# Kernel optimization log

Measured on AMD Instinct MI355X. Metric: run time of the kernel, lower is better.

Reference implementation:

```python
import jax, jax.numpy as jnp
import numpy as np
from jax import lax

K = 9      # 3x3 kernel points
PAD = 1
EPS = 1e-5

def _conv3x3(x, w):
    # x: [B,C,H,W], w: [O,C,3,3] -> [B,O,H,W], stride 1, pad 1
    return lax.conv_general_dilated(x, w, (1, 1), [(PAD, PAD), (PAD, PAD)],
                                    dimension_numbers=('NCHW', 'OIHW', 'NCHW'))

def _bilinear_sample(x, py, px):
    # x: [B,C,H,W]; py,px: [B,K,H,W] float sample coords -> [B,C,K,H,W]
    # Zero padding outside bounds (mmcv deform_conv semantics).
    B, C, H, W = x.shape
    y0 = jnp.floor(py)
    x0 = jnp.floor(px)
    wy1 = py - y0
    wx1 = px - x0
    xf = x.reshape(B, C, H * W)

    def corner(yc, xc, wgt):
        valid = (yc >= 0) & (yc <= H - 1) & (xc >= 0) & (xc <= W - 1)
        yi = jnp.clip(yc, 0, H - 1).astype(jnp.int32)
        xi = jnp.clip(xc, 0, W - 1).astype(jnp.int32)
        idx = (yi * W + xi).reshape(B, -1)                       # [B, K*H*W]
        v = jax.vmap(lambda f, i: jnp.take(f, i, axis=1))(xf, idx)  # [B,C,K*H*W]
        v = v.reshape(B, C, K, H, W)
        return v * jnp.where(valid, wgt, 0.0)[:, None]

    return (corner(y0,     x0,     (1 - wy1) * (1 - wx1))
          + corner(y0,     x0 + 1, (1 - wy1) * wx1)
          + corner(y0 + 1, x0,     wy1 * (1 - wx1))
          + corner(y0 + 1, x0 + 1, wy1 * wx1))

def _dcn_bn_relu(x, w_off, b_off, w, gamma, beta, mean, var):
    B, C, H, W = x.shape
    # offset conv: [B, 2K, H, W]; channel pairs are (dy, dx) per kernel point
    off = _conv3x3(x, w_off) + b_off[None, :, None, None]
    off = off.reshape(B, K, 2, H, W)
    dy, dx = off[:, :, 0], off[:, :, 1]
    kk = jnp.arange(K)
    ky = (kk // 3 - PAD).astype(x.dtype)   # kernel y deltas
    kx = (kk % 3 - PAD).astype(x.dtype)    # kernel x deltas
    py = dy + jnp.arange(H, dtype=x.dtype)[None, None, :, None] + ky[None, :, None, None]
    px = dx + jnp.arange(W, dtype=x.dtype)[None, None, None, :] + kx[None, :, None, None]
    s = _bilinear_sample(x, py, px)                       # [B,C,K,H,W]
    out = jnp.einsum('bckhw,ock->bohw', s, w.reshape(w.shape[0], C, K))
    # BatchNorm (eval stats) + ReLU
    inv = gamma * lax.rsqrt(var + EPS)
    return jax.nn.relu(out * inv[None, :, None, None]
                       + (beta - mean * inv)[None, :, None, None])

def setup_inputs() -> dict:
    key = jax.random.key(0)
    ks = jax.random.split(key, 8)
    B, Cin, Cout, H, W = 4, 64, 64, 128, 128
    fan = 1.0 / np.sqrt(Cin * K)
    return {
        'x':      jax.random.normal(ks[0], (B, Cin, H, W), jnp.float32),
        'w_off1': jax.random.normal(ks[1], (2 * K, Cin, 3, 3), jnp.float32) * 0.1,
        'b_off1': jnp.zeros((2 * K,), jnp.float32),
        'w1':     jax.random.normal(ks[2], (Cout, Cin, 3, 3), jnp.float32) * fan,
        'g1':     jnp.ones((Cout,), jnp.float32),
        'be1':    jnp.zeros((Cout,), jnp.float32),
        'm1':     jax.random.normal(ks[3], (Cout,), jnp.float32) * 0.01,
        'v1':     jnp.abs(jax.random.normal(ks[4], (Cout,), jnp.float32)) * 0.1 + 0.9,
        'w_off2': jax.random.normal(ks[5], (2 * K, Cout, 3, 3), jnp.float32) * 0.1,
        'b_off2': jnp.zeros((2 * K,), jnp.float32),
        'w2':     jax.random.normal(ks[6], (Cout, Cout, 3, 3), jnp.float32) * fan,
        'g2':     jnp.ones((Cout,), jnp.float32),
        'be2':    jnp.zeros((Cout,), jnp.float32),
        'm2':     jax.random.normal(ks[7], (Cout,), jnp.float32) * 0.01,
        'v2':     jnp.ones((Cout,), jnp.float32),
    }

def reference(x, w_off1, b_off1, w1, g1, be1, m1, v1,
              w_off2, b_off2, w2, g2, be2, m2, v2):
    h = _dcn_bn_relu(x, w_off1, b_off1, w1, g1, be1, m1, v1)
    return _dcn_bn_relu(h, w_off2, b_off2, w2, g2, be2, m2, v2)
```

## Files before the change

kernel.cpp:

```cpp
#include <hip/hip_runtime.h>

#define BAR_LGKM()                                         \
  do {                                                     \
    asm volatile("s_waitcnt lgkmcnt(0)" ::: "memory");     \
    __builtin_amdgcn_s_barrier();                          \
  } while (0)

__device__ __forceinline__ int swz_block(int bid) {
  return ((bid & 7) << 7) + (bid >> 3);
}


__global__ __launch_bounds__(256) void prep_kernel(
    const float* __restrict__ w1, const float* __restrict__ w2,
    const float* __restrict__ woff1, const float* __restrict__ woff2,
    const float* __restrict__ g1, const float* __restrict__ be1,
    const float* __restrict__ m1, const float* __restrict__ v1,
    const float* __restrict__ g2, const float* __restrict__ be2,
    const float* __restrict__ m2, const float* __restrict__ v2,
    float* __restrict__ ws) {
  float* wt1 = ws;
  float* wt2 = ws + 36864;
  float* wo1 = ws + 73728;
  float* wo2 = ws + 84096;
  float* bn1 = ws + 94464;
  float* bn2 = ws + 94592;
  int idx = blockIdx.x * 256 + threadIdx.x;
  if (idx < 73728) {
    int t = (idx < 36864) ? idx : idx - 36864;
    const float* w = (idx < 36864) ? w1 : w2;
    float* wt = (idx < 36864) ? wt1 : wt2;
    int oi = t & 7;
    int rest = t >> 3;
    int k = rest % 9;
    int cog = rest / 9;
    int og = cog & 7, c = cog >> 3;
    int o = og * 8 + oi;
    wt[t] = w[(o * 64 + c) * 9 + k];
  } else if (idx < 94464) {
    int u = idx - 73728;
    int t2 = (u < 10368) ? u : u - 10368;
    const float* w = (u < 10368) ? woff1 : woff2;
    float* wo = (u < 10368) ? wo1 : wo2;
    int j = t2 % 18;
    int v = t2 / 18;
    int tt = v % 9;
    int c = v / 9;
    wo[t2] = w[(j * 64 + c) * 9 + tt];
  } else if (idx < 94528) {
    int o = idx - 94464;
    float s = g1[o] * rsqrtf(v1[o] + 1e-5f);
    bn1[o] = s;
    bn1[64 + o] = be1[o] - m1[o] * s;
  } else if (idx < 94592) {
    int o = idx - 94528;
    float s = g2[o] * rsqrtf(v2[o] + 1e-5f);
    bn2[o] = s;
    bn2[64 + o] = be2[o] - m2[o] * s;
  }
}

__global__ __launch_bounds__(512, 8) void conv_off_kernel(
    const float* __restrict__ xin, const float* __restrict__ wofft,
    const float* __restrict__ boff, float* __restrict__ off) {
  __shared__ float halo[2][792];
  int tid = threadIdx.x;
  int pxl = tid & 63;
  int og = tid >> 6;
  int ogu = __builtin_amdgcn_readfirstlane(og);
  int p0 = swz_block(blockIdx.x) * 64;
  int b = p0 >> 14, hw0 = p0 & 16383;
  int h = hw0 >> 7, w0 = hw0 & 127;

  bool sv = tid < 396;
  int pp = (tid >= 198) ? 1 : 0;
  int pos = tid - pp * 198;
  int r = pos / 66, cc = pos - r * 66;
  int yy = h + r - 1, xx = w0 + cc - 1;
  bool inb = sv && (yy >= 0) && (yy < 128) && (xx >= 0) && (xx < 128);
  int ofs = (yy << 7) + xx;
  const float* xb0 = xin + ((size_t)(b * 64) << 14);

  float stg0 = inb ? xb0[((size_t)pp << 14) + ofs] : 0.f;
  float stg1 = inb ? xb0[((size_t)(2 + pp) << 14) + ofs] : 0.f;

  int jbase = (ogu < 2) ? ogu * 3 : 6 + (ogu - 2) * 2;
  int nj = (ogu < 2) ? 3 : 2;
  int jc2 = jbase + 2;
  if (jc2 > 17) jc2 = 17;

  float acc[3] = {0.f, 0.f, 0.f};

#pragma unroll 1
  for (int cg = 0; cg < 64; cg += 4) {
    int bufi = (cg >> 2) & 1;
    if (sv) {
      halo[bufi][pp * 198 + pos] = stg0;
      halo[bufi][(2 + pp) * 198 + pos] = stg1;
    }
    if (cg < 60) {
      stg0 = inb ? xb0[((size_t)(cg + 4 + pp) << 14) + ofs] : 0.f;
      stg1 = inb ? xb0[((size_t)(cg + 6 + pp) << 14) + ofs] : 0.f;
    }
    BAR_LGKM();
    const float* hb = halo[bufi];
#pragma unroll
    for (int p = 0; p < 4; ++p) {
      const float* wc = wofft + (cg + p) * 162;
#pragma unroll
      for (int t = 0; t < 9; ++t) {
        float v = hb[p * 198 + (t / 3) * 66 + pxl + (t % 3)];
        acc[0] = fmaf(v, wc[t * 18 + jbase], acc[0]);
        acc[1] = fmaf(v, wc[t * 18 + jbase + 1], acc[1]);
        acc[2] = fmaf(v, wc[t * 18 + jc2], acc[2]);
      }
    }
  }
#pragma unroll
  for (int i = 0; i < 3; ++i) {
    if (i < nj) {
      int j = jbase + i;
      off[((size_t)(b * 18 + j) << 14) + hw0 + pxl] = acc[i] + boff[j];
    }
  }
}

__global__ __launch_bounds__(512, 8) void dcn_main_kernel(
    const float* __restrict__ xin, const float* __restrict__ off,
    const float* __restrict__ wt, const float* __restrict__ bn,
    float* __restrict__ out) {
  __shared__ float sbuf[2][576];
  int tid = threadIdx.x;
  int pxl = tid & 63;
  int og = tid >> 6;
  int ogu = __builtin_amdgcn_readfirstlane(og);
  int p0 = swz_block(blockIdx.x) * 64;
  int b = p0 >> 14, hw0 = p0 & 16383;
  int h = hw0 >> 7, w0 = hw0 & 127;
  const float* xb = xin + ((size_t)b << 20);

  bool act1 = (tid & 7) == 0;
  int s1 = 512 + (tid >> 3);

  float q[2][4];
  const float* pa[2];
  const float* pb[2];

#pragma unroll
  for (int j = 0; j < 2; ++j) {
    bool a = (j == 0) || act1;
    int s = (j == 0) ? tid : s1;
    int k = s >> 6;
    int pxs = s & 63;
    int hw = hw0 + pxs;
    float dy = a ? off[((size_t)(b * 18 + 2 * k) << 14) + hw] : 0.f;
    float dx = a ? off[((size_t)(b * 18 + 2 * k + 1) << 14) + hw] : 0.f;
    float py = (float)(h + k / 3 - 1) + dy;
    float pxf = (float)(w0 + pxs + k % 3 - 1) + dx;
    float y0f = floorf(py), x0f = floorf(pxf);
    float wy1 = py - y0f, wx1 = pxf - x0f;
    float wy0 = 1.f - wy1, wx0 = 1.f - wx1;
    int y0 = (int)y0f, x0 = (int)x0f;
    int y1 = y0 + 1, x1 = x0 + 1;
    bool vy0 = (y0 >= 0) && (y0 <= 127);
    bool vy1 = (y1 >= 0) && (y1 <= 127);
    bool vx0 = (x0 >= 0) && (x0 <= 127);
    bool vx1 = (x1 >= 0) && (x1 <= 127);
    float pw0 = (vy0 && vx0) ? wy0 * wx0 : 0.f;
    float pw1 = (vy0 && vx1) ? wy0 * wx1 : 0.f;
    float pw2 = (vy1 && vx0) ? wy1 * wx0 : 0.f;
    float pw3 = (vy1 && vx1) ? wy1 * wx1 : 0.f;
    int y0c = min(max(y0, 0), 127), y1c = min(max(y1, 0), 127);
    int xb2 = min(max(x0, 0), 126);
    bool se0 = (x0 == xb2);
    bool se1 = (x0 + 1 == xb2);
    q[j][0] = (se0 ? pw0 : 0.f) + (se1 ? pw1 : 0.f);
    q[j][1] = (se0 ? 0.f : pw0) + (se1 ? 0.f : pw1);
    q[j][2] = (se0 ? pw2 : 0.f) + (se1 ? pw3 : 0.f);
    q[j][3] = (se0 ? 0.f : pw2) + (se1 ? 0.f : pw3);
    pa[j] = xb + ((y0c << 7) + xb2);
    pb[j] = xb + ((y1c << 7) + xb2);
  }

  float2 t0a = *(const float2*)pa[0];
  float2 t1a = *(const float2*)pb[0];
  float2 t0b = act1 ? *(const float2*)pa[1] : make_float2(0.f, 0.f);
  float2 t1b = act1 ? *(const float2*)pb[1] : make_float2(0.f, 0.f);
  pa[0] += 16384; pb[0] += 16384; pa[1] += 16384; pb[1] += 16384;

  float acc[8];
#pragma unroll
  for (int oi = 0; oi < 8; ++oi) acc[oi] = 0.f;

#pragma unroll 1
  for (int c = 0; c < 64; ++c) {
    sbuf[c & 1][tid] = fmaf(q[0][0], t0a.x,
                       fmaf(q[0][1], t0a.y,
                       fmaf(q[0][2], t1a.x, q[0][3] * t1a.y)));
    if (act1) {
      sbuf[c & 1][s1] = fmaf(q[1][0], t0b.x,
                        fmaf(q[1][1], t0b.y,
                        fmaf(q[1][2], t1b.x, q[1][3] * t1b.y)));
    }
    if (c < 63) {
      t0a = *(const float2*)pa[0];
      t1a = *(const float2*)pb[0];
      if (act1) {
        t0b = *(const float2*)pa[1];
        t1b = *(const float2*)pb[1];
      }
      pa[0] += 16384; pb[0] += 16384; pa[1] += 16384; pb[1] += 16384;
    }
    BAR_LGKM();
    const float* wc = wt + (c * 8 + ogu) * 72;
#pragma unroll
    for (int k = 0; k < 9; ++k) {
      float sval = sbuf[c & 1][k * 64 + pxl];
#pragma unroll
      for (int oi = 0; oi < 8; ++oi)
        acc[oi] = fmaf(sval, wc[k * 8 + oi], acc[oi]);
    }
  }

#pragma unroll
  for (int oi = 0; oi < 8; ++oi) {
    int o = ogu * 8 + oi;
    float rres = fmaf(acc[oi], bn[o], bn[64 + o]);
    out[((size_t)(b * 64 + o) << 14) + hw0 + pxl] = fmaxf(rres, 0.f);
  }
}

extern "C" void kernel_launch(void* const* d_in, const int* in_sizes, int n_in,
                              void* d_out, int out_size, void* d_ws, size_t ws_size,
                              hipStream_t stream) {
  const float* x      = (const float*)d_in[0];
  const float* w_off1 = (const float*)d_in[1];
  const float* b_off1 = (const float*)d_in[2];
  const float* w1     = (const float*)d_in[3];
  const float* g1     = (const float*)d_in[4];
  const float* be1    = (const float*)d_in[5];
  const float* m1     = (const float*)d_in[6];
  const float* v1     = (const float*)d_in[7];
  const float* w_off2 = (const float*)d_in[8];
  const float* b_off2 = (const float*)d_in[9];
  const float* w2     = (const float*)d_in[10];
  const float* g2     = (const float*)d_in[11];
  const float* be2    = (const float*)d_in[12];
  const float* m2     = (const float*)d_in[13];
  const float* v2     = (const float*)d_in[14];
  float* out = (float*)d_out;

  float* ws   = (float*)d_ws;
  float* wt1  = ws;
  float* wt2  = ws + 36864;
  float* wo1  = ws + 73728;
  float* wo2  = ws + 84096;
  float* bn1  = ws + 94464;
  float* bn2  = ws + 94592;
  float* offb = ws + 94720;
  float* hbuf = ws + 1274368;

  prep_kernel<<<370, 256, 0, stream>>>(w1, w2, w_off1, w_off2,
                                       g1, be1, m1, v1, g2, be2, m2, v2, ws);

  conv_off_kernel<<<1024, 512, 0, stream>>>(x, wo1, b_off1, offb);
  dcn_main_kernel<<<1024, 512, 0, stream>>>(x, offb, wt1, bn1, hbuf);

  conv_off_kernel<<<1024, 512, 0, stream>>>(hbuf, wo2, b_off2, offb);
  dcn_main_kernel<<<1024, 512, 0, stream>>>(hbuf, offb, wt2, bn2, out);
}
```

Baseline: 375.5 us.

## Stage input halo tile in LDS and software-pipeline sampling with weight accumulation

Each block now cooperatively loads a 17x80 halo window of the current input channel into double-buffered shared memory. Bilinear corner values are read from LDS when the sample lies inside the window, and from global memory only when it falls outside. The loop is also restructured so the FMA accumulation for channel c-1 overlaps the sampling for channel c, with one barrier per iteration. This replaces scattered global gathers with coalesced loads, at the cost of more LDS per block, lower launch-bound occupancy, and divergent fallback loads when offsets are large.

```diff
diff --git a/kernel.cpp b/kernel.cpp
--- a/kernel.cpp
+++ b/kernel.cpp
@@ -125,10 +125,11 @@
   }
 }
 
-__global__ __launch_bounds__(512, 8) void dcn_main_kernel(
+__global__ __launch_bounds__(512, 6) void dcn_main_kernel(
     const float* __restrict__ xin, const float* __restrict__ off,
     const float* __restrict__ wt, const float* __restrict__ bn,
     float* __restrict__ out) {
+  __shared__ float xs[2][1360];
   __shared__ float sbuf[2][576];
   int tid = threadIdx.x;
   int pxl = tid & 63;
@@ -142,15 +143,29 @@
   bool act1 = (tid & 7) == 0;
   int s1 = 512 + (tid >> 3);
 
-  float q[2][4];
-  const float* pa[2];
-  const float* pb[2];
+  int h0 = h - 8, xlo = w0 - 8;
+
+  int sofs[3]; bool svld[3];
+#pragma unroll
+  for (int i = 0; i < 3; ++i) {
+    int e = tid + i * 512;
+    int r = e / 80, col = e - r * 80;
+    int y = h0 + r, xc = xlo + col;
+    svld[i] = (e < 1360) && (y >= 0) && (y < 128) && (xc >= 0) && (xc < 128);
+    sofs[i] = (y << 7) + xc;
+  }
+
+  float qa[2][2], qb[2][2];
+  int lA[2], lB[2];
+  int ra[2], rb[2];
+  bool ina[2], inb[2];
 
 #pragma unroll
   for (int j = 0; j < 2; ++j) {
     bool a = (j == 0) || act1;
     int s = (j == 0) ? tid : s1;
     int k = s >> 6;
+    if (k > 8) k = 8;
     int pxs = s & 63;
     int hw = hw0 + pxs;
     float dy = a ? off[((size_t)(b * 18 + 2 * k) << 14) + hw] : 0.f;
@@ -174,51 +189,97 @@
     int xb2 = min(max(x0, 0), 126);
     bool se0 = (x0 == xb2);
     bool se1 = (x0 + 1 == xb2);
-    q[j][0] = (se0 ? pw0 : 0.f) + (se1 ? pw1 : 0.f);
-    q[j][1] = (se0 ? 0.f : pw0) + (se1 ? 0.f : pw1);
-    q[j][2] = (se0 ? pw2 : 0.f) + (se1 ? pw3 : 0.f);
-    q[j][3] = (se0 ? 0.f : pw2) + (se1 ? 0.f : pw3);
-    pa[j] = xb + ((y0c << 7) + xb2);
-    pb[j] = xb + ((y1c << 7) + xb2);
-  }
-
-  float2 t0a = *(const float2*)pa[0];
-  float2 t1a = *(const float2*)pb[0];
-  float2 t0b = act1 ? *(const float2*)pa[1] : make_float2(0.f, 0.f);
-  float2 t1b = act1 ? *(const float2*)pb[1] : make_float2(0.f, 0.f);
-  pa[0] += 16384; pb[0] += 16384; pa[1] += 16384; pb[1] += 16384;
+    float f0 = (se0 ? pw0 : 0.f) + (se1 ? pw1 : 0.f);
+    float f1 = (se0 ? 0.f : pw0) + (se1 ? 0.f : pw1);
+    float f2 = (se0 ? pw2 : 0.f) + (se1 ? pw3 : 0.f);
+    float f3 = (se0 ? 0.f : pw2) + (se1 ? 0.f : pw3);
+    int ry = y0 - h0, rx = x0 - xlo;
+    bool inx = (rx >= 0) && (rx <= 78);
+    bool iA = inx && (ry >= 0) && (ry <= 16);
+    bool iB = inx && (ry >= -1) && (ry <= 15);
+    int la = ry * 80 + rx;
+    lA[j] = min(max(la, 0), 1358);
+    lB[j] = min(max(la + 80, 0), 1358);
+    ina[j] = iA;
+    inb[j] = iB;
+    qa[j][0] = iA ? pw0 : f0;  qa[j][1] = iA ? pw1 : f1;
+    qb[j][0] = iB ? pw2 : f2;  qb[j][1] = iB ? pw3 : f3;
+    ra[j] = (y0c << 7) + xb2;
+    rb[j] = (y1c << 7) + xb2;
+  }
+
+  {
+    float a0 = svld[0] ? xb[sofs[0]] : 0.f;
+    float a1 = svld[1] ? xb[sofs[1]] : 0.f;
+    float a2 = svld[2] ? xb[sofs[2]] : 0.f;
+    xs[0][tid] = a0;
+    xs[0][tid + 512] = a1;
+    if (tid < 336) xs[0][tid + 1024] = a2;
+  }
 
   float acc[8];
 #pragma unroll
   for (int oi = 0; oi < 8; ++oi) acc[oi] = 0.f;
+
+  BAR_LGKM();
 
 #pragma unroll 1
   for (int c = 0; c < 64; ++c) {
-    sbuf[c & 1][tid] = fmaf(q[0][0], t0a.x,
-                       fmaf(q[0][1], t0a.y,
-                       fmaf(q[0][2], t1a.x, q[0][3] * t1a.y)));
+    int buf = c & 1;
+    const float* xp = xb + ((size_t)c << 14);
+    float n0 = 0.f, n1 = 0.f, n2 = 0.f;
+    if (c < 63) {
+      const float* xq = xp + 16384;
+      n0 = svld[0] ? xq[sofs[0]] : 0.f;
+      n1 = svld[1] ? xq[sofs[1]] : 0.f;
+      n2 = svld[2] ? xq[sofs[2]] : 0.f;
+    }
+    const float* xsb = xs[buf];
+    {
+      float vax = xsb[lA[0]], vay = xsb[lA[0] + 1];
+      float vbx = xsb[lB[0]], vby = xsb[lB[0] + 1];
+      if (!ina[0]) { float2 t = *(const float2*)(xp + ra[0]); vax = t.x; vay = t.y; }
+      if (!inb[0]) { float2 t = *(const float2*)(xp + rb[0]); vbx = t.x; vby = t.y; }
+      sbuf[buf][tid] = fmaf(qa[0][0], vax, fmaf(qa[0][1], vay,
+                        fmaf(qb[0][0], vbx, qb[0][1] * vby)));
+    }
     if (act1) {
-      sbuf[c & 1][s1] = fmaf(q[1][0], t0b.x,
-                        fmaf(q[1][1], t0b.y,
-                        fmaf(q[1][2], t1b.x, q[1][3] * t1b.y)));
+      float vax = xsb[lA[1]], vay = xsb[lA[1] + 1];
+      float vbx = xsb[lB[1]], vby = xsb[lB[1] + 1];
+      if (!ina[1]) { float2 t = *(const float2*)(xp + ra[1]); vax = t.x; vay = t.y; }
+      if (!inb[1]) { float2 t = *(const float2*)(xp + rb[1]); vbx = t.x; vby = t.y; }
+      sbuf[buf][s1] = fmaf(qa[1][0], vax, fmaf(qa[1][1], vay,
+                       fmaf(qb[1][0], vbx, qb[1][1] * vby)));
+    }
+    if (c > 0) {
+      const float* wc = wt + ((c - 1) * 8 + ogu) * 72;
+      const float* sb = sbuf[buf ^ 1];
+#pragma unroll
+      for (int k = 0; k < 9; ++k) {
+        float sv_ = sb[k * 64 + pxl];
+#pragma unroll
+        for (int oi = 0; oi < 8; ++oi)
+          acc[oi] = fmaf(sv_, wc[k * 8 + oi], acc[oi]);
+      }
     }
     if (c < 63) {
-      t0a = *(const float2*)pa[0];
-      t1a = *(const float2*)pb[0];
-      if (act1) {
-        t0b = *(const float2*)pa[1];
-        t1b = *(const float2*)pb[1];
-      }
-      pa[0] += 16384; pb[0] += 16384; pa[1] += 16384; pb[1] += 16384;
+      float* xd = xs[buf ^ 1];
+      xd[tid] = n0;
+      xd[tid + 512] = n1;
+      if (tid < 336) xd[tid + 1024] = n2;
     }
     BAR_LGKM();
-    const float* wc = wt + (c * 8 + ogu) * 72;
+  }
+
+  {
+    const float* wc = wt + (63 * 8 + ogu) * 72;
+    const float* sb = sbuf[1];
 #pragma unroll
     for (int k = 0; k < 9; ++k) {
-      float sval = sbuf[c & 1][k * 64 + pxl];
+      float sv_ = sb[k * 64 + pxl];
 #pragma unroll
       for (int oi = 0; oi < 8; ++oi)
-        acc[oi] = fmaf(sval, wc[k * 8 + oi], acc[oi]);
+        acc[oi] = fmaf(sv_, wc[k * 8 + oi], acc[oi]);
     }
   }
 
```

After: 469.7 us. 25.1% more time.

## Use split-bf16 MFMA for deformable conv GEMM instead of scalar FMA

Applied to the files above, without the earlier changes.

The main DCN kernel's channel-by-kernel-point reduction moves from per-thread scalar FMAs to bf16 MFMA 16x16x32 instructions. Both the sampled activations and the weights are split into high and low bf16 parts, and three MFMAs (hi*hi, hi*lo, lo*hi) recover near-fp32 accuracy. The prep kernel repacks weights into an MFMA-friendly hi/lo bf16 layout padded from 9 to 16 per channel. Two channels are packed per K=32 step with double-buffered LDS. The cost is the padding waste and the extra split arithmetic, plus a lower occupancy hint.

```diff
diff --git a/kernel.cpp b/kernel.cpp
--- a/kernel.cpp
+++ b/kernel.cpp
@@ -5,6 +5,11 @@
     asm volatile("s_waitcnt lgkmcnt(0)" ::: "memory");     \
     __builtin_amdgcn_s_barrier();                          \
   } while (0)
+
+typedef __attribute__((ext_vector_type(8))) short bf16x8;
+typedef __attribute__((ext_vector_type(4))) float f32x4;
+typedef unsigned short u16;
+typedef unsigned int u32;
 
 __device__ __forceinline__ int swz_block(int bid) {
   return ((bid & 7) << 7) + (bid >> 3);
@@ -19,26 +24,38 @@
     const float* __restrict__ g2, const float* __restrict__ be2,
     const float* __restrict__ m2, const float* __restrict__ v2,
     float* __restrict__ ws) {
-  float* wt1 = ws;
-  float* wt2 = ws + 36864;
-  float* wo1 = ws + 73728;
-  float* wo2 = ws + 84096;
-  float* bn1 = ws + 94464;
-  float* bn2 = ws + 94592;
+  u16* wm1 = (u16*)ws;
+  u16* wm2 = (u16*)(ws + 65536);
+  float* wo1 = ws + 131072;
+  float* wo2 = ws + 141440;
+  float* bn1 = ws + 151808;
+  float* bn2 = ws + 151936;
   int idx = blockIdx.x * 256 + threadIdx.x;
-  if (idx < 73728) {
-    int t = (idx < 36864) ? idx : idx - 36864;
-    const float* w = (idx < 36864) ? w1 : w2;
-    float* wt = (idx < 36864) ? wt1 : wt2;
-    int oi = t & 7;
-    int rest = t >> 3;
-    int k = rest % 9;
-    int cog = rest / 9;
-    int og = cog & 7, c = cog >> 3;
-    int o = og * 8 + oi;
-    wt[t] = w[(o * 64 + c) * 9 + k];
-  } else if (idx < 94464) {
-    int u = idx - 73728;
+  if (idx < 131072) {
+    int t = idx & 65535;
+    const float* w = (idx < 65536) ? w1 : w2;
+    u16* wm = (idx < 65536) ? wm1 : wm2;
+    int i = t & 7;
+    int lane = (t >> 3) & 63;
+    int nt = (t >> 9) & 3;
+    int pair = t >> 11;
+    int k = ((lane >> 4) << 3) + i;
+    int c = (pair << 1) + (k >> 4);
+    int kk = k & 15;
+    int o = (nt << 4) + (lane & 15);
+    float val = (kk < 9) ? w[(o * 64 + c) * 9 + kk] : 0.f;
+    u32 u = __float_as_uint(val);
+    u32 r = u + 0x7FFFu + ((u >> 16) & 1u);
+    u16 hi = (u16)(r >> 16);
+    float lo = val - __uint_as_float(((u32)hi) << 16);
+    u32 u2 = __float_as_uint(lo);
+    u32 r2 = u2 + 0x7FFFu + ((u2 >> 16) & 1u);
+    u16 lov = (u16)(r2 >> 16);
+    size_t base = ((size_t)(pair * 4 + nt) * 2) * 512 + lane * 8 + i;
+    wm[base] = hi;
+    wm[base + 512] = lov;
+  } else if (idx < 151808) {
+    int u = idx - 131072;
     int t2 = (u < 10368) ? u : u - 10368;
     const float* w = (u < 10368) ? woff1 : woff2;
     float* wo = (u < 10368) ? wo1 : wo2;
@@ -47,13 +64,13 @@
     int tt = v % 9;
     int c = v / 9;
     wo[t2] = w[(j * 64 + c) * 9 + tt];
-  } else if (idx < 94528) {
-    int o = idx - 94464;
+  } else if (idx < 151872) {
+    int o = idx - 151808;
     float s = g1[o] * rsqrtf(v1[o] + 1e-5f);
     bn1[o] = s;
     bn1[64 + o] = be1[o] - m1[o] * s;
-  } else if (idx < 94592) {
-    int o = idx - 94528;
+  } else if (idx < 151936) {
+    int o = idx - 151872;
     float s = g2[o] * rsqrtf(v2[o] + 1e-5f);
     bn2[o] = s;
     bn2[64 + o] = be2[o] - m2[o] * s;
@@ -125,22 +142,26 @@
   }
 }
 
-__global__ __launch_bounds__(512, 8) void dcn_main_kernel(
+__global__ __launch_bounds__(512, 6) void dcn_main_kernel(
     const float* __restrict__ xin, const float* __restrict__ off,
-    const float* __restrict__ wt, const float* __restrict__ bn,
+    const float* __restrict__ wmf, const float* __restrict__ bn,
     float* __restrict__ out) {
-  __shared__ float sbuf[2][576];
+  __shared__ __align__(16) u16 Ah[2][64][40];
+  __shared__ __align__(16) u16 Al[2][64][40];
+  __shared__ __align__(16) u16 Bs[2][4096];
   int tid = threadIdx.x;
-  int pxl = tid & 63;
-  int og = tid >> 6;
-  int ogu = __builtin_amdgcn_readfirstlane(og);
+  int lane = tid & 63;
+  int wv = tid >> 6;
+  int wvu = __builtin_amdgcn_readfirstlane(wv);
   int p0 = swz_block(blockIdx.x) * 64;
   int b = p0 >> 14, hw0 = p0 & 16383;
   int h = hw0 >> 7, w0 = hw0 & 127;
   const float* xb = xin + ((size_t)b << 20);
+  const u16* wmu = (const u16*)wmf;
 
   bool act1 = (tid & 7) == 0;
   int s1 = 512 + (tid >> 3);
+  int px1 = tid >> 3;
 
   float q[2][4];
   const float* pa[2];
@@ -182,25 +203,54 @@
     pb[j] = xb + ((y1c << 7) + xb2);
   }
 
+  for (int z = tid; z < 3584; z += 512) {
+    int m = z / 896;
+    int rr = z - m * 896;
+    int px = rr / 14, jj = rr - (rr / 14) * 14;
+    int k = (jj < 7) ? (9 + jj) : (18 + jj);
+    u16* bp = (m < 2) ? &Ah[m][0][0] : &Al[m - 2][0][0];
+    bp[px * 40 + k] = 0;
+  }
+
   float2 t0a = *(const float2*)pa[0];
   float2 t1a = *(const float2*)pb[0];
   float2 t0b = act1 ? *(const float2*)pa[1] : make_float2(0.f, 0.f);
   float2 t1b = act1 ? *(const float2*)pb[1] : make_float2(0.f, 0.f);
   pa[0] += 16384; pb[0] += 16384; pa[1] += 16384; pb[1] += 16384;
 
-  float acc[8];
-#pragma unroll
-  for (int oi = 0; oi < 8; ++oi) acc[oi] = 0.f;
+  int mt = wvu >> 1;
+  int ntb = (wvu & 1) * 2;
+  int apx = mt * 16 + (lane & 15);
+  int akf = (lane >> 4) * 8;
+
+  f32x4 acc0 = {0.f, 0.f, 0.f, 0.f};
+  f32x4 acc1 = {0.f, 0.f, 0.f, 0.f};
+  uint4 bst = make_uint4(0, 0, 0, 0);
 
 #pragma unroll 1
   for (int c = 0; c < 64; ++c) {
-    sbuf[c & 1][tid] = fmaf(q[0][0], t0a.x,
-                       fmaf(q[0][1], t0a.y,
-                       fmaf(q[0][2], t1a.x, q[0][3] * t1a.y)));
+    int pbW = (c >> 1) & 1;
+    int kh = (c & 1) << 4;
+    {
+      float s = fmaf(q[0][0], t0a.x, fmaf(q[0][1], t0a.y,
+                fmaf(q[0][2], t1a.x, q[0][3] * t1a.y)));
+      u32 u = __float_as_uint(s);
+      Ah[pbW][lane][kh + wv] = (u16)(u >> 16);
+      float lo = s - __uint_as_float(u & 0xFFFF0000u);
+      Al[pbW][lane][kh + wv] = (u16)(__float_as_uint(lo) >> 16);
+    }
     if (act1) {
-      sbuf[c & 1][s1] = fmaf(q[1][0], t0b.x,
-                        fmaf(q[1][1], t0b.y,
-                        fmaf(q[1][2], t1b.x, q[1][3] * t1b.y)));
+      float s = fmaf(q[1][0], t0b.x, fmaf(q[1][1], t0b.y,
+                fmaf(q[1][2], t1b.x, q[1][3] * t1b.y)));
+      u32 u = __float_as_uint(s);
+      Ah[pbW][px1][kh + 8] = (u16)(u >> 16);
+      float lo = s - __uint_as_float(u & 0xFFFF0000u);
+      Al[pbW][px1][kh + 8] = (u16)(__float_as_uint(lo) >> 16);
+    }
+    if (!(c & 1)) {
+      bst = *(const uint4*)(wmu + (size_t)(c >> 1) * 4096 + tid * 8);
+    } else {
+      *(uint4*)&Bs[pbW][tid * 8] = bst;
     }
     if (c < 63) {
       t0a = *(const float2*)pa[0];
@@ -212,21 +262,33 @@
       pa[0] += 16384; pb[0] += 16384; pa[1] += 16384; pb[1] += 16384;
     }
     BAR_LGKM();
-    const float* wc = wt + (c * 8 + ogu) * 72;
-#pragma unroll
-    for (int k = 0; k < 9; ++k) {
-      float sval = sbuf[c & 1][k * 64 + pxl];
-#pragma unroll
-      for (int oi = 0; oi < 8; ++oi)
-        acc[oi] = fmaf(sval, wc[k * 8 + oi], acc[oi]);
-    }
-  }
-
-#pragma unroll
-  for (int oi = 0; oi < 8; ++oi) {
-    int o = ogu * 8 + oi;
-    float rres = fmaf(acc[oi], bn[o], bn[64 + o]);
-    out[((size_t)(b * 64 + o) << 14) + hw0 + pxl] = fmaxf(rres, 0.f);
+    if (c & 1) {
+      bf16x8 ah = *(const bf16x8*)&Ah[pbW][apx][akf];
+      bf16x8 al = *(const bf16x8*)&Al[pbW][apx][akf];
+      const u16* bsp = &Bs[pbW][0];
+      bf16x8 b0h = *(const bf16x8*)(bsp + (ntb * 2 + 0) * 512 + lane * 8);
+      bf16x8 b0l = *(const bf16x8*)(bsp + (ntb * 2 + 1) * 512 + lane * 8);
+      bf16x8 b1h = *(const bf16x8*)(bsp + (ntb * 2 + 2) * 512 + lane * 8);
+      bf16x8 b1l = *(const bf16x8*)(bsp + (ntb * 2 + 3) * 512 + lane * 8);
+      acc0 = __builtin_amdgcn_mfma_f32_16x16x32_bf16(ah, b0h, acc0, 0, 0, 0);
+      acc1 = __builtin_amdgcn_mfma_f32_16x16x32_bf16(ah, b1h, acc1, 0, 0, 0);
+      acc0 = __builtin_amdgcn_mfma_f32_16x16x32_bf16(ah, b0l, acc0, 0, 0, 0);
+      acc1 = __builtin_amdgcn_mfma_f32_16x16x32_bf16(ah, b1l, acc1, 0, 0, 0);
+      acc0 = __builtin_amdgcn_mfma_f32_16x16x32_bf16(al, b0h, acc0, 0, 0, 0);
+      acc1 = __builtin_amdgcn_mfma_f32_16x16x32_bf16(al, b1h, acc1, 0, 0, 0);
+    }
+  }
+
+  int o0 = ntb * 16 + (lane & 15);
+  int prow = mt * 16 + ((lane >> 4) << 2);
+  float sc0 = bn[o0], sh0 = bn[64 + o0];
+  float sc1 = bn[16 + o0], sh1 = bn[80 + o0];
+  float* ob0 = out + (((size_t)(b * 64 + o0)) << 14) + hw0 + prow;
+  float* ob1 = out + (((size_t)(b * 64 + o0 + 16)) << 14) + hw0 + prow;
+#pragma unroll
+  for (int r = 0; r < 4; ++r) {
+    ob0[r] = fmaxf(fmaf(acc0[r], sc0, sh0), 0.f);
+    ob1[r] = fmaxf(fmaf(acc1[r], sc1, sh1), 0.f);
   }
 }
 
@@ -251,21 +313,21 @@
   float* out = (float*)d_out;
 
   float* ws   = (float*)d_ws;
-  float* wt1  = ws;
-  float* wt2  = ws + 36864;
-  float* wo1  = ws + 73728;
-  float* wo2  = ws + 84096;
-  float* bn1  = ws + 94464;
-  float* bn2  = ws + 94592;
-  float* offb = ws + 94720;
-  float* hbuf = ws + 1274368;
-
-  prep_kernel<<<370, 256, 0, stream>>>(w1, w2, w_off1, w_off2,
+  float* wm1  = ws;
+  float* wm2  = ws + 65536;
+  float* wo1  = ws + 131072;
+  float* wo2  = ws + 141440;
+  float* bn1  = ws + 151808;
+  float* bn2  = ws + 151936;
+  float* offb = ws + 152064;
+  float* hbuf = ws + 1331712;
+
+  prep_kernel<<<594, 256, 0, stream>>>(w1, w2, w_off1, w_off2,
                                        g1, be1, m1, v1, g2, be2, m2, v2, ws);
 
   conv_off_kernel<<<1024, 512, 0, stream>>>(x, wo1, b_off1, offb);
-  dcn_main_kernel<<<1024, 512, 0, stream>>>(x, offb, wt1, bn1, hbuf);
+  dcn_main_kernel<<<1024, 512, 0, stream>>>(x, offb, wm1, bn1, hbuf);
 
   conv_off_kernel<<<1024, 512, 0, stream>>>(hbuf, wo2, b_off2, offb);
-  dcn_main_kernel<<<1024, 512, 0, stream>>>(hbuf, offb, wt2, bn2, out);
-}
+  dcn_main_kernel<<<1024, 512, 0, stream>>>(hbuf, offb, wm2, bn2, out);
+}
```

New measurement: 392.8 us. +4.6%, slower.

## Bucket-sort deformable sample points by source row to coalesce gathers

Applied to the files above, without the earlier changes.

Before the channel loop, the kernel stages per-sample bilinear coefficients and indices in shared memory. It then builds a histogram of source rows, relative to the output row, and uses a counting sort to reassign sample points to threads. Threads in a wavefront then gather from nearby rows, which should improve cache-line coalescing of the per-channel gathers, and results are written back to the original sbuf slot. The cost is extra LDS (about 16 KB), atomics and several block barriers, which may reduce occupancy under the 8-blocks launch bound.

```diff
diff --git a/kernel.cpp b/kernel.cpp
--- a/kernel.cpp
+++ b/kernel.cpp
@@ -129,6 +129,9 @@
     const float* __restrict__ xin, const float* __restrict__ off,
     const float* __restrict__ wt, const float* __restrict__ bn,
     float* __restrict__ out) {
+  __shared__ float prm[576 * 6];
+  __shared__ int sortmap[576];
+  __shared__ int hist[32];
   __shared__ float sbuf[2][576];
   int tid = threadIdx.x;
   int pxl = tid & 63;
@@ -142,10 +145,9 @@
   bool act1 = (tid & 7) == 0;
   int s1 = 512 + (tid >> 3);
 
-  float q[2][4];
-  const float* pa[2];
-  const float* pb[2];
-
+  if (tid < 32) hist[tid] = 0;
+
+  int bkt[2];
 #pragma unroll
   for (int j = 0; j < 2; ++j) {
     bool a = (j == 0) || act1;
@@ -174,12 +176,57 @@
     int xb2 = min(max(x0, 0), 126);
     bool se0 = (x0 == xb2);
     bool se1 = (x0 + 1 == xb2);
-    q[j][0] = (se0 ? pw0 : 0.f) + (se1 ? pw1 : 0.f);
-    q[j][1] = (se0 ? 0.f : pw0) + (se1 ? 0.f : pw1);
-    q[j][2] = (se0 ? pw2 : 0.f) + (se1 ? pw3 : 0.f);
-    q[j][3] = (se0 ? 0.f : pw2) + (se1 ? 0.f : pw3);
-    pa[j] = xb + ((y0c << 7) + xb2);
-    pb[j] = xb + ((y1c << 7) + xb2);
+    float f0 = (se0 ? pw0 : 0.f) + (se1 ? pw1 : 0.f);
+    float f1 = (se0 ? 0.f : pw0) + (se1 ? 0.f : pw1);
+    float f2 = (se0 ? pw2 : 0.f) + (se1 ? pw3 : 0.f);
+    float f3 = (se0 ? 0.f : pw2) + (se1 ? 0.f : pw3);
+    if (a) {
+      float* pp = &prm[s * 6];
+      pp[0] = f0; pp[1] = f1; pp[2] = f2; pp[3] = f3;
+      ((int*)pp)[4] = (y0c << 7) + xb2;
+      ((int*)pp)[5] = (y1c << 7) + xb2;
+    }
+    bkt[j] = min(max(y0 - (h - 10), 0), 20);
+  }
+  __syncthreads();
+  atomicAdd(&hist[bkt[0]], 1);
+  if (act1) atomicAdd(&hist[bkt[1]], 1);
+  __syncthreads();
+  if (tid == 0) {
+    int run = 0;
+#pragma unroll 1
+    for (int i = 0; i <= 20; ++i) { int t = hist[i]; hist[i] = run; run += t; }
+  }
+  __syncthreads();
+  {
+    int r0 = atomicAdd(&hist[bkt[0]], 1);
+    sortmap[r0] = tid;
+    if (act1) {
+      int r1 = atomicAdd(&hist[bkt[1]], 1);
+      sortmap[r1] = s1;
+    }
+  }
+  __syncthreads();
+
+  int ws0 = sortmap[tid];
+  int ws1 = act1 ? sortmap[512 + (tid >> 3)] : 0;
+  float q[2][4];
+  const float* pa[2];
+  const float* pb[2];
+  {
+    const float* pp = &prm[ws0 * 6];
+    q[0][0] = pp[0]; q[0][1] = pp[1]; q[0][2] = pp[2]; q[0][3] = pp[3];
+    pa[0] = xb + ((const int*)pp)[4];
+    pb[0] = xb + ((const int*)pp)[5];
+  }
+  if (act1) {
+    const float* pp = &prm[ws1 * 6];
+    q[1][0] = pp[0]; q[1][1] = pp[1]; q[1][2] = pp[2]; q[1][3] = pp[3];
+    pa[1] = xb + ((const int*)pp)[4];
+    pb[1] = xb + ((const int*)pp)[5];
+  } else {
+    q[1][0] = q[1][1] = q[1][2] = q[1][3] = 0.f;
+    pa[1] = xb; pb[1] = xb;
   }
 
   float2 t0a = *(const float2*)pa[0];
@@ -194,13 +241,13 @@
 
 #pragma unroll 1
   for (int c = 0; c < 64; ++c) {
-    sbuf[c & 1][tid] = fmaf(q[0][0], t0a.x,
+    sbuf[c & 1][ws0] = fmaf(q[0][0], t0a.x,
                        fmaf(q[0][1], t0a.y,
                        fmaf(q[0][2], t1a.x, q[0][3] * t1a.y)));
     if (act1) {
-      sbuf[c & 1][s1] = fmaf(q[1][0], t0b.x,
-                        fmaf(q[1][1], t0b.y,
-                        fmaf(q[1][2], t1b.x, q[1][3] * t1b.y)));
+      sbuf[c & 1][ws1] = fmaf(q[1][0], t0b.x,
+                         fmaf(q[1][1], t0b.y,
+                         fmaf(q[1][2], t1b.x, q[1][3] * t1b.y)));
     }
     if (c < 63) {
       t0a = *(const float2*)pa[0];
```

Result: faster. 335.8 us (-10.6%).
